# Kernel tuning notes

Hardware: AMD Instinct MI355X
Metric: run time of the kernel (lower is better)

## Reference

```python
import jax, jax.numpy as jnp
import numpy as np

B_, S_, H_, I_, N_, K_ = 2, 2048, 1024, 2048, 16, 4

def setup_inputs() -> dict:
    key = jax.random.key(0)
    ks = jax.random.split(key, 6)
    return {
        "x": jax.random.normal(ks[0], (B_, S_, H_), jnp.float32),
        "W_in": jax.random.normal(ks[1], (H_, 2 * I_), jnp.float32) * (H_ ** -0.5),
        "conv_w": jax.random.normal(ks[2], (I_, 1, K_), jnp.float32) * (K_ ** -0.5),
        "ln_gamma": jnp.ones((I_,), jnp.float32),
        "ln_beta": jnp.zeros((I_,), jnp.float32),
        "W_xproj": jax.random.normal(ks[3], (I_, 2 * N_ + 1), jnp.float32) * (I_ ** -0.5),
        "A_param": jax.random.normal(ks[4], (I_, N_), jnp.float32) * 0.1,
        "D": jnp.ones((I_,), jnp.float32),
        "W_out": jax.random.normal(ks[5], (I_, H_), jnp.float32) * (I_ ** -0.5),
    }

def _layernorm(x, g, b, eps=1e-5):
    mu = jnp.mean(x, axis=-1, keepdims=True)
    var = jnp.mean((x - mu) ** 2, axis=-1, keepdims=True)
    return (x - mu) * jax.lax.rsqrt(var + eps) * g + b

def reference(x, W_in, conv_w, ln_gamma, ln_beta, W_xproj, A_param, D, W_out):
    b, s, _ = x.shape
    n = A_param.shape[1]
    xz = x @ W_in                                   # (b,s,2I)
    xc, z = jnp.split(xz, 2, axis=-1)
    # depthwise causal conv1d: torch pads both sides k-1 then truncates [:s] == left-pad k-1
    xc = jax.lax.conv_general_dilated(
        xc.transpose(0, 2, 1), conv_w, window_strides=(1,),
        padding=[(conv_w.shape[-1] - 1, 0)],
        feature_group_count=conv_w.shape[0],
        dimension_numbers=("NCH", "OIH", "NCH")).transpose(0, 2, 1)  # (b,s,I)
    xc = jax.nn.silu(xc)
    xc = _layernorm(xc, ln_gamma, ln_beta)
    xp = xc @ W_xproj                               # (b,s,2N+1)
    delta = jnp.clip(jax.nn.softplus(xp[..., :1]), 1e-6, 10.0)   # (b,s,1)
    Bm = xp[..., 1:1 + n]                           # (b,s,N)
    Cm = xp[..., 1 + n:]                            # (b,s,N)
    A = -jnp.clip(jax.nn.softplus(A_param), 0.1, 10.0)           # (I,N)
    # decay[b,s,i,n] = exp(delta[b,s] * A[i,n]), clamped
    decay = jnp.clip(jnp.exp(delta[..., None] * A[None, None]), 1e-6, 1.0)  # (b,s,I,N)
    # y = x * sum_n B*C*decay  (state-dim reduction of the broadcast 4D tensor)
    y = xc * jnp.einsum("bsn,bsin->bsi", Bm * Cm, decay)
    y = y + xc * D
    return (y * jax.nn.silu(z)) @ W_out
```

## Files before the change

### kernel.cpp

```cpp
#include <hip/hip_runtime.h>
#include <hip/hip_bf16.h>
#include <cmath>

typedef __bf16 bf16_t;
typedef __bf16 bf16x8 __attribute__((ext_vector_type(8)));
typedef __bf16 bf16x4 __attribute__((ext_vector_type(4)));
typedef float  f32x4  __attribute__((ext_vector_type(4)));

static constexpr int B_  = 2, S_ = 2048, H_ = 1024, I_ = 2048, NST = 16;
static constexpr int ROWS  = B_ * S_;
static constexpr int TWO_I = 2 * I_;
static constexpr int XPD   = 2 * NST + 1;
static constexpr int XPN   = 64;

#define AS_G(p) ((const __attribute__((address_space(1))) void*)(p))
#define AS_L(p) ((__attribute__((address_space(3))) void*)(p))

template<int N> __device__ __forceinline__ void wait_vmcnt();
template<> __device__ __forceinline__ void wait_vmcnt<4>() {
    asm volatile("s_waitcnt vmcnt(4)" ::: "memory");
}

__device__ __forceinline__ float softplus_f(float x) {
    return x > 15.f ? x : log1pf(__expf(x));
}

__device__ __forceinline__ f32x4 b2f(bf16x4 v) {
    return (f32x4){(float)v[0], (float)v[1], (float)v[2], (float)v[3]};
}

__device__ __forceinline__ float fast_exp2(float x) {
#if __has_builtin(__builtin_amdgcn_exp2f)
    return __builtin_amdgcn_exp2f(x);
#else
    return exp2f(x);
#endif
}
__device__ __forceinline__ float fast_rcp(float x) {
#if __has_builtin(__builtin_amdgcn_rcpf)
    return __builtin_amdgcn_rcpf(x);
#else
    return 1.f / x;
#endif
}
__device__ __forceinline__ float fast_sigmoid(float x) {
    return fast_rcp(1.f + __expf(-x));
}
__device__ __forceinline__ float rflf(float x) {
    return __int_as_float(__builtin_amdgcn_readfirstlane(__float_as_int(x)));
}

template<int GX, int GY, int XW>
__device__ __forceinline__ void xcd_swz(int id, int& bx, int& by) {
    constexpr int SX = GX / XW;
    constexpr int SY = GY * XW / 8;
    const int xcd = id & 7;
    const int j   = id >> 3;
    bx = (xcd % XW) * SX + j % SX;
    by = (xcd / XW) * SY + j / SX;
}


__global__ __launch_bounds__(256)
void prep_all(const float* __restrict__ x, const float* __restrict__ W_in,
              const float* __restrict__ W_out, const float* __restrict__ A_param,
              const float* __restrict__ Wx, const float* __restrict__ conv_w,
              bf16_t* __restrict__ Xb, bf16_t* __restrict__ W1t,
              bf16_t* __restrict__ Wot, float* __restrict__ A2T,
              float* __restrict__ cwT, bf16_t* __restrict__ WxTb)
{
    const int b   = blockIdx.x;
    const int tid = threadIdx.x;
    __shared__ float t[32][33];

    if (b < 4096) {
        const int i = b * 256 + tid;
        f32x4 v = *(const f32x4*)(x + (size_t)i * 4);
        bf16x4 o;
        o[0] = (bf16_t)v[0]; o[1] = (bf16_t)v[1];
        o[2] = (bf16_t)v[2]; o[3] = (bf16_t)v[3];
        *(bf16x4*)(Xb + (size_t)i * 4) = o;
    } else if (b < 8192) {
        const int tb = b - 4096;
        const int c0 = (tb & 127) * 32, r0 = (tb >> 7) * 32;
        const int tx = tid & 31, ty = tid >> 5;
        #pragma unroll
        for (int k = 0; k < 4; ++k)
            t[ty + 8 * k][tx] = W_in[(size_t)(r0 + ty + 8 * k) * 4096 + c0 + tx];
        __syncthreads();
        #pragma unroll
        for (int k = 0; k < 4; ++k)
            W1t[(size_t)(c0 + ty + 8 * k) * 1024 + r0 + tx] = (bf16_t)t[tx][ty + 8 * k];
    } else if (b < 10240) {
        const int tb = b - 8192;
        const int c0 = (tb & 31) * 32, r0 = (tb >> 5) * 32;
        const int tx = tid & 31, ty = tid >> 5;
        #pragma unroll
        for (int k = 0; k < 4; ++k)
            t[ty + 8 * k][tx] = W_out[(size_t)(r0 + ty + 8 * k) * 1024 + c0 + tx];
        __syncthreads();
        #pragma unroll
        for (int k = 0; k < 4; ++k)
            Wot[(size_t)(c0 + ty + 8 * k) * 2048 + r0 + tx] = (bf16_t)t[tx][ty + 8 * k];
    } else {
        const int i = (b - 10240) * 256 + tid;
        if (i < NST * I_) {
            int n = i >> 11, c = i & (I_ - 1);
            float sp = softplus_f(A_param[(size_t)c * NST + n]);
            A2T[i] = -fminf(fmaxf(sp, 0.1f), 10.f) * 1.44269504088896340736f;
        }
        if (i < 4 * I_) {
            int j = i >> 11, c = i & (I_ - 1);
            cwT[i] = conv_w[(size_t)c * 4 + j];
        }
        if (i < XPN * I_) {
            int j = i >> 11, c = i & (I_ - 1);
            WxTb[i] = (j < XPD) ? (bf16_t)Wx[(size_t)c * XPD + j] : (bf16_t)0.f;
        }
    }
}


template<int M, int N, int K, int BM, int BN, int WM, int WN, int THREADS,
         int GX, int GY, int XW, typename OutT>
__global__ __launch_bounds__(THREADS)
void gemm_fp(const bf16_t* __restrict__ A, const bf16_t* __restrict__ Bt,
             OutT* __restrict__ C)
{
    constexpr int BK  = 32;
    constexpr int NT  = K / BK;
    constexpr int MR  = BM / WM / 16;
    constexpr int NR  = BN / WN / 16;
    constexpr int MH  = MR / 2;
    constexpr int RPC = THREADS / 4;
    constexpr int CA  = BM / RPC;
    constexpr int CB  = BN / RPC;
    static_assert(CA + CB == 4, "vmcnt template fixed at 4");

    __shared__ bf16_t lA[4][BM * BK];
    __shared__ bf16_t lB[4][BN * BK];

    int bx, by;
    xcd_swz<GX, GY, XW>(blockIdx.x, bx, by);
    const int bm = by * BM;
    const int bn = bx * BN;

    const int tid  = threadIdx.x;
    const int lane = tid & 63;
    const int wave = tid >> 6;
    const int wm   = wave / WN;
    const int wn   = wave % WN;

    const int frow = lane & 15;
    const int fsw  = ((lane >> 4) ^ ((frow >> 1) & 3)) << 3;

    const int str = tid >> 2;
    const int stp = tid & 3;

    const bf16_t* baseA[CA];
    #pragma unroll
    for (int a = 0; a < CA; ++a) {
        const int rt = a * RPC + str;
        baseA[a] = A + (size_t)(bm + rt) * K + ((stp ^ ((rt >> 1) & 3)) << 3);
    }
    const bf16_t* baseB[CB];
    #pragma unroll
    for (int a = 0; a < CB; ++a) {
        const int rt = a * RPC + str;
        baseB[a] = Bt + (size_t)(bn + rt) * K + ((stp ^ ((rt >> 1) & 3)) << 3);
    }

    f32x4 acc[MR][NR];
    #pragma unroll
    for (int m = 0; m < MR; ++m)
        #pragma unroll
        for (int n = 0; n < NR; ++n)
            acc[m][n] = (f32x4){0.f, 0.f, 0.f, 0.f};

    auto stageA = [&](int k0, int b) {
        #pragma unroll
        for (int a = 0; a < CA; ++a)
            __builtin_amdgcn_global_load_lds(AS_G(baseA[a] + k0),
                AS_L(&lA[b][a * RPC * 32 + wave * 512]), 16, 0, 0);
    };
    auto stageB = [&](int k0, int b) {
        #pragma unroll
        for (int a = 0; a < CB; ++a)
            __builtin_amdgcn_global_load_lds(AS_G(baseB[a] + k0),
                AS_L(&lB[b][a * RPC * 32 + wave * 512]), 16, 0, 0);
    };

    stageA(0, 0); stageB(0, 0);
    stageA(BK, 1); stageB(BK, 1);
    wait_vmcnt<4>();
    __builtin_amdgcn_s_barrier();

    #pragma unroll 1
    for (int t = 0; t < NT; ++t) {
        const int buf = t & 3;
        const int nb  = (t + 2) & 3;
        int kn = (t + 2) * BK;
        if (kn >= K) kn -= K;

        bf16x8 bfr[NR];
        #pragma unroll
        for (int n = 0; n < NR; ++n)
            bfr[n] = *(const bf16x8*)(&lB[buf][(wn * (NR * 16) + n * 16 + frow) * 32 + fsw]);
        bf16x8 af0[MH];
        #pragma unroll
        for (int m = 0; m < MH; ++m)
            af0[m] = *(const bf16x8*)(&lA[buf][(wm * (MR * 16) + m * 16 + frow) * 32 + fsw]);
        stageA(kn, nb);

        __builtin_amdgcn_s_setprio(1);
        #pragma unroll
        for (int m = 0; m < MH; ++m)
            #pragma unroll
            for (int n = 0; n < NR; ++n)
                acc[m][n] = __builtin_amdgcn_mfma_f32_16x16x32_bf16(
                    af0[m], bfr[n], acc[m][n], 0, 0, 0);
        __builtin_amdgcn_s_setprio(0);

        bf16x8 af1[MR - MH];
        #pragma unroll
        for (int m = 0; m < MR - MH; ++m)
            af1[m] = *(const bf16x8*)(&lA[buf][(wm * (MR * 16) + (MH + m) * 16 + frow) * 32 + fsw]);
        stageB(kn, nb);

        __builtin_amdgcn_s_setprio(1);
        #pragma unroll
        for (int m = 0; m < MR - MH; ++m)
            #pragma unroll
            for (int n = 0; n < NR; ++n)
                acc[MH + m][n] = __builtin_amdgcn_mfma_f32_16x16x32_bf16(
                    af1[m], bfr[n], acc[MH + m][n], 0, 0, 0);
        __builtin_amdgcn_s_setprio(0);

        wait_vmcnt<4>();
        __builtin_amdgcn_s_barrier();
    }

    const int crow = (lane >> 4) * 4;
    const int ccol = lane & 15;
    #pragma unroll
    for (int m = 0; m < MR; ++m)
        #pragma unroll
        for (int n = 0; n < NR; ++n)
            #pragma unroll
            for (int r = 0; r < 4; ++r)
                C[(size_t)(bm + wm * (MR * 16) + m * 16 + crow + r) * N
                  + (bn + wn * (NR * 16) + n * 16 + ccol)] = (OutT)acc[m][n][r];
}


template<int M, int N, int K, int GX, int GY, int XW>
__global__ __launch_bounds__(512)
void gemm3_kg(const bf16_t* __restrict__ A, const bf16_t* __restrict__ Bt,
              float* __restrict__ C)
{
    constexpr int BM = 128, BN = 128, BK = 32;
    constexpr int KH = K / 2;
    constexpr int NT = KH / BK;
    constexpr int MR = 4, NR = 4, MH = 2;

    __shared__ bf16_t smem[65536];

    int bx, by;
    xcd_swz<GX, GY, XW>(blockIdx.x, bx, by);
    const int bm = by * BM;
    const int bn = bx * BN;

    const int tid  = threadIdx.x;
    const int lane = tid & 63;
    const int wave = tid >> 6;
    const int grp  = wave >> 2;
    const int gw   = wave & 3;
    const int wm   = gw >> 1;
    const int wn   = gw & 1;

    const int frow = lane & 15;
    const int fsw  = ((lane >> 4) ^ ((frow >> 1) & 3)) << 3;

    const int gtid = tid & 255;
    const int str  = gtid >> 2;
    const int stp  = gtid & 3;

    bf16_t* lA = smem + grp * 16384;
    bf16_t* lB = smem + 32768 + grp * 16384;

    const bf16_t* baseA[2];
    #pragma unroll
    for (int a = 0; a < 2; ++a) {
        const int rt = a * 64 + str;
        baseA[a] = A + (size_t)(bm + rt) * K + grp * KH + ((stp ^ ((rt >> 1) & 3)) << 3);
    }
    const bf16_t* baseB[2];
    #pragma unroll
    for (int a = 0; a < 2; ++a) {
        const int rt = a * 64 + str;
        baseB[a] = Bt + (size_t)(bn + rt) * K + grp * KH + ((stp ^ ((rt >> 1) & 3)) << 3);
    }

    f32x4 acc[MR][NR];
    #pragma unroll
    for (int m = 0; m < MR; ++m)
        #pragma unroll
        for (int n = 0; n < NR; ++n)
            acc[m][n] = (f32x4){0.f, 0.f, 0.f, 0.f};

    auto stageA = [&](int k0, int b) {
        #pragma unroll
        for (int a = 0; a < 2; ++a)
            __builtin_amdgcn_global_load_lds(AS_G(baseA[a] + k0),
                AS_L(lA + b * 4096 + a * 2048 + gw * 512), 16, 0, 0);
    };
    auto stageB = [&](int k0, int b) {
        #pragma unroll
        for (int a = 0; a < 2; ++a)
            __builtin_amdgcn_global_load_lds(AS_G(baseB[a] + k0),
                AS_L(lB + b * 4096 + a * 2048 + gw * 512), 16, 0, 0);
    };

    stageA(0, 0); stageB(0, 0);
    stageA(BK, 1); stageB(BK, 1);
    wait_vmcnt<4>();
    __builtin_amdgcn_s_barrier();

    #pragma unroll 1
    for (int t = 0; t < NT; ++t) {
        const int buf = t & 3;
        const int nb  = (t + 2) & 3;
        int kn = (t + 2) * BK;
        if (kn >= KH) kn -= KH;

        bf16x8 bfr[NR];
        #pragma unroll
        for (int n = 0; n < NR; ++n)
            bfr[n] = *(const bf16x8*)(lB + buf * 4096 + (wn * 64 + n * 16 + frow) * 32 + fsw);
        bf16x8 af0[MH];
        #pragma unroll
        for (int m = 0; m < MH; ++m)
            af0[m] = *(const bf16x8*)(lA + buf * 4096 + (wm * 64 + m * 16 + frow) * 32 + fsw);
        stageA(kn, nb);

        __builtin_amdgcn_s_setprio(1);
        #pragma unroll
        for (int m = 0; m < MH; ++m)
            #pragma unroll
            for (int n = 0; n < NR; ++n)
                acc[m][n] = __builtin_amdgcn_mfma_f32_16x16x32_bf16(
                    af0[m], bfr[n], acc[m][n], 0, 0, 0);
        __builtin_amdgcn_s_setprio(0);

        bf16x8 af1[MR - MH];
        #pragma unroll
        for (int m = 0; m < MR - MH; ++m)
            af1[m] = *(const bf16x8*)(lA + buf * 4096 + (wm * 64 + (MH + m) * 16 + frow) * 32 + fsw);
        stageB(kn, nb);

        __builtin_amdgcn_s_setprio(1);
        #pragma unroll
        for (int m = 0; m < MR - MH; ++m)
            #pragma unroll
            for (int n = 0; n < NR; ++n)
                acc[MH + m][n] = __builtin_amdgcn_mfma_f32_16x16x32_bf16(
                    af1[m], bfr[n], acc[MH + m][n], 0, 0, 0);
        __builtin_amdgcn_s_setprio(0);

        wait_vmcnt<4>();
        __builtin_amdgcn_s_barrier();
    }

    asm volatile("s_waitcnt vmcnt(0)" ::: "memory");
    __builtin_amdgcn_s_barrier();

    float* accx = (float*)smem;
    const int crow = (lane >> 4) * 4;
    const int ccol = lane & 15;

    if (grp == 1) {
        #pragma unroll
        for (int m = 0; m < MR; ++m)
            #pragma unroll
            for (int n = 0; n < NR; ++n) {
                const int row = wm * 64 + m * 16 + crow;
                const int col = wn * 64 + n * 16 + ccol;
                #pragma unroll
                for (int r = 0; r < 4; ++r)
                    accx[(size_t)(row + r) * 132 + col] = acc[m][n][r];
            }
    }
    __syncthreads();
    if (grp == 0) {
        #pragma unroll
        for (int m = 0; m < MR; ++m)
            #pragma unroll
            for (int n = 0; n < NR; ++n) {
                const int row = wm * 64 + m * 16 + crow;
                const int col = wn * 64 + n * 16 + ccol;
                #pragma unroll
                for (int r = 0; r < 4; ++r)
                    C[(size_t)(bm + row + r) * N + bn + col] =
                        acc[m][n][r] + accx[(size_t)(row + r) * 132 + col];
            }
    }
}


__global__ __launch_bounds__(256)
void conv_ln(const bf16_t* __restrict__ xz,
             const float* __restrict__ cwT,
             const float* __restrict__ ln_g,
             const float* __restrict__ ln_b,
             bf16_t* __restrict__ Xn)
{
    const int row  = blockIdx.x;
    const int s    = row & (S_ - 1);
    const int tid  = threadIdx.x;
    const int lane = tid & 63;
    const int wave = tid >> 6;
    const bf16_t* xzr = xz + (size_t)row * TWO_I;

    __shared__ float lnr[4][2];

    float xc[8];
    float sm = 0.f, sq = 0.f;

    #pragma unroll
    for (int g = 0; g < 2; ++g) {
        const int c = g * 1024 + tid * 4;
        const f32x4 w0 = *(const f32x4*)(cwT + 0 * I_ + c);
        const f32x4 w1 = *(const f32x4*)(cwT + 1 * I_ + c);
        const f32x4 w2 = *(const f32x4*)(cwT + 2 * I_ + c);
        const f32x4 w3 = *(const f32x4*)(cwT + 3 * I_ + c);
        const f32x4 z4 = (f32x4){0.f, 0.f, 0.f, 0.f};
        const f32x4 xv0 = (s >= 3) ? b2f(*(const bf16x4*)(xzr - 3 * TWO_I + c)) : z4;
        const f32x4 xv1 = (s >= 2) ? b2f(*(const bf16x4*)(xzr - 2 * TWO_I + c)) : z4;
        const f32x4 xv2 = (s >= 1) ? b2f(*(const bf16x4*)(xzr - 1 * TWO_I + c)) : z4;
        const f32x4 xv3 = b2f(*(const bf16x4*)(xzr + c));
        const f32x4 a = w0 * xv0 + w1 * xv1 + w2 * xv2 + w3 * xv3;
        #pragma unroll
        for (int e = 0; e < 4; ++e) {
            const float v = a[e];
            const float t = v * fast_sigmoid(v);
            xc[g * 4 + e] = t;
            sm += t; sq += t * t;
        }
    }

    #pragma unroll
    for (int off = 32; off; off >>= 1) {
        sm += __shfl_xor(sm, off, 64);
        sq += __shfl_xor(sq, off, 64);
    }
    if (lane == 0) { lnr[wave][0] = sm; lnr[wave][1] = sq; }
    __syncthreads();
    sm = lnr[0][0] + lnr[1][0] + lnr[2][0] + lnr[3][0];
    sq = lnr[0][1] + lnr[1][1] + lnr[2][1] + lnr[3][1];
    const float mu = sm * (1.f / I_);
    const float rs = rsqrtf(sq * (1.f / I_) - mu * mu + 1e-5f);

    #pragma unroll
    for (int g = 0; g < 2; ++g) {
        const int c = g * 1024 + tid * 4;
        const f32x4 gg = *(const f32x4*)(ln_g + c);
        const f32x4 bb = *(const f32x4*)(ln_b + c);
        bf16x4 h4;
        #pragma unroll
        for (int e = 0; e < 4; ++e)
            h4[e] = (bf16_t)((xc[g * 4 + e] - mu) * rs * gg[e] + bb[e]);
        *(bf16x4*)(Xn + (size_t)row * I_ + c) = h4;
    }
}


__global__ __launch_bounds__(256)
void xproj_gemm(const bf16_t* __restrict__ Xn,
                const bf16_t* __restrict__ Wb, float* __restrict__ xp_part)
{
    constexpr int BM = 128, BK = 32, KS = 512;
    __shared__ bf16_t lA[BM * BK];
    __shared__ bf16_t lB[XPN * BK];

    const int bm   = blockIdx.x * BM;
    const int ks   = blockIdx.y;
    const int tid  = threadIdx.x;
    const int lane = tid & 63;
    const int wave = tid >> 6;
    const int wm   = (wave >> 1) * 64;
    const int wn   = (wave & 1) * 32;

    const int srow  = lane >> 2;
    const int skoff = (lane & 3) * 8;
    const int frow  = lane & 15;
    const int fko   = (lane >> 4) * 8;

    f32x4 acc[4][2];
    #pragma unroll
    for (int m = 0; m < 4; ++m)
        #pragma unroll
        for (int n = 0; n < 2; ++n)
            acc[m][n] = (f32x4){0.f, 0.f, 0.f, 0.f};

    for (int k0 = ks * KS; k0 < ks * KS + KS; k0 += BK) {
        #pragma unroll
        for (int t = 0; t < 2; ++t) {
            const int c = wave * 2 + t;
            const bf16_t* ga = Xn + (size_t)(bm + c * 16 + srow) * I_ + k0 + skoff;
            __builtin_amdgcn_global_load_lds(AS_G(ga), AS_L(lA + c * 512), 16, 0, 0);
        }
        const bf16_t* gb = Wb + (size_t)(wave * 16 + srow) * I_ + k0 + skoff;
        __builtin_amdgcn_global_load_lds(AS_G(gb), AS_L(lB + wave * 512), 16, 0, 0);
        __syncthreads();

        bf16x8 af[4], bf2[2];
        #pragma unroll
        for (int m = 0; m < 4; ++m)
            af[m] = *(const bf16x8*)(lA + (wm + m * 16 + frow) * BK + fko);
        #pragma unroll
        for (int n = 0; n < 2; ++n)
            bf2[n] = *(const bf16x8*)(lB + (wn + n * 16 + frow) * BK + fko);

        #pragma unroll
        for (int m = 0; m < 4; ++m)
            #pragma unroll
            for (int n = 0; n < 2; ++n)
                acc[m][n] = __builtin_amdgcn_mfma_f32_16x16x32_bf16(
                    af[m], bf2[n], acc[m][n], 0, 0, 0);

        __syncthreads();
    }

    float* out = xp_part + ((size_t)ks * ROWS + bm) * XPN;
    const int crow = (lane >> 4) * 4;
    const int ccol = lane & 15;
    #pragma unroll
    for (int m = 0; m < 4; ++m)
        #pragma unroll
        for (int n = 0; n < 2; ++n)
            #pragma unroll
            for (int r = 0; r < 4; ++r)
                out[(size_t)(wm + m * 16 + crow + r) * XPN
                    + (wn + n * 16 + ccol)] = acc[m][n][r];
}


__global__ __launch_bounds__(256)
void ssm_gate(const bf16_t* __restrict__ xz,
              const bf16_t* __restrict__ Xn,
              const float* __restrict__ xp_part,
              const float* __restrict__ A2T,
              const float* __restrict__ Dv,
              bf16_t* __restrict__ U)
{
    const int row0 = blockIdx.x * 2;
    const int tid  = threadIdx.x;

    __shared__ float xps[2][XPD];
    __shared__ float bcs[2][NST];

    if (tid < XPD) {
        float s = 0.f;
        #pragma unroll
        for (int ks = 0; ks < 4; ++ks)
            s += xp_part[((size_t)ks * ROWS + row0) * XPN + tid];
        xps[0][tid] = s;
    } else if (tid >= 64 && tid < 64 + XPD) {
        const int j = tid - 64;
        float s = 0.f;
        #pragma unroll
        for (int ks = 0; ks < 4; ++ks)
            s += xp_part[((size_t)ks * ROWS + row0 + 1) * XPN + j];
        xps[1][j] = s;
    }
    __syncthreads();
    if (tid < NST)
        bcs[0][tid] = xps[0][1 + tid] * xps[0][1 + NST + tid];
    else if (tid >= 64 && tid < 64 + NST) {
        const int n = tid - 64;
        bcs[1][n] = xps[1][1 + n] * xps[1][1 + NST + n];
    }
    __syncthreads();

    const float d0 = fminf(fmaxf(softplus_f(xps[0][0]), 1e-6f), 10.f);
    const float d1 = fminf(fmaxf(softplus_f(xps[1][0]), 1e-6f), 10.f);

    const bf16_t* z0 = xz + (size_t)row0 * TWO_I + I_;
    const bf16_t* z1 = z0 + TWO_I;
    bf16_t* u0 = U + (size_t)row0 * I_;
    bf16_t* u1 = u0 + I_;

    #pragma unroll 1
    for (int g = 0; g < 2; ++g) {
        const int c = g * 1024 + tid * 4;
        f32x4 sa0 = (f32x4){0.f, 0.f, 0.f, 0.f};
        f32x4 sa1 = (f32x4){0.f, 0.f, 0.f, 0.f};
        #pragma unroll 1
        for (int nb = 0; nb < 4; ++nb) {
            const float* ap = A2T + (size_t)(nb * 4) * I_ + c;
            const f32x4 a0 = *(const f32x4*)(ap);
            const f32x4 a1 = *(const f32x4*)(ap + I_);
            const f32x4 a2 = *(const f32x4*)(ap + 2 * I_);
            const f32x4 a3 = *(const f32x4*)(ap + 3 * I_);
            const float b00 = rflf(bcs[0][nb * 4 + 0]), b10 = rflf(bcs[1][nb * 4 + 0]);
            const float b01 = rflf(bcs[0][nb * 4 + 1]), b11 = rflf(bcs[1][nb * 4 + 1]);
            const float b02 = rflf(bcs[0][nb * 4 + 2]), b12 = rflf(bcs[1][nb * 4 + 2]);
            const float b03 = rflf(bcs[0][nb * 4 + 3]), b13 = rflf(bcs[1][nb * 4 + 3]);
            #pragma unroll
            for (int e = 0; e < 4; ++e) {
                sa0[e] += b00 * fast_exp2(d0 * a0[e]);
                sa1[e] += b10 * fast_exp2(d1 * a0[e]);
                sa0[e] += b01 * fast_exp2(d0 * a1[e]);
                sa1[e] += b11 * fast_exp2(d1 * a1[e]);
                sa0[e] += b02 * fast_exp2(d0 * a2[e]);
                sa1[e] += b12 * fast_exp2(d1 * a2[e]);
                sa0[e] += b03 * fast_exp2(d0 * a3[e]);
                sa1[e] += b13 * fast_exp2(d1 * a3[e]);
            }
        }
        const f32x4 dvv = *(const f32x4*)(Dv + c);
        const f32x4 xn0 = b2f(*(const bf16x4*)(Xn + (size_t)row0 * I_ + c));
        const f32x4 xn1 = b2f(*(const bf16x4*)(Xn + (size_t)(row0 + 1) * I_ + c));
        const f32x4 zv0 = b2f(*(const bf16x4*)(z0 + c));
        const f32x4 zv1 = b2f(*(const bf16x4*)(z1 + c));
        bf16x4 o0, o1;
        #pragma unroll
        for (int e = 0; e < 4; ++e) {
            const float y0 = xn0[e] * (sa0[e] + dvv[e]);
            const float y1 = xn1[e] * (sa1[e] + dvv[e]);
            const float zz0 = zv0[e], zz1 = zv1[e];
            o0[e] = (bf16_t)(y0 * zz0 * fast_sigmoid(zz0));
            o1[e] = (bf16_t)(y1 * zz1 * fast_sigmoid(zz1));
        }
        *(bf16x4*)(u0 + c) = o0;
        *(bf16x4*)(u1 + c) = o1;
    }
}


extern "C" void kernel_launch(void* const* d_in, const int* in_sizes, int n_in,
                              void* d_out, int out_size, void* d_ws, size_t ws_size,
                              hipStream_t stream)
{
    const float* x     = (const float*)d_in[0];
    const float* W_in  = (const float*)d_in[1];
    const float* convw = (const float*)d_in[2];
    const float* ln_g  = (const float*)d_in[3];
    const float* ln_b  = (const float*)d_in[4];
    const float* Wx    = (const float*)d_in[5];
    const float* A_p   = (const float*)d_in[6];
    const float* Dv    = (const float*)d_in[7];
    const float* W_out = (const float*)d_in[8];
    float* out = (float*)d_out;

    char* ws = (char*)d_ws;
    bf16_t* Xb   = (bf16_t*)(ws);
    bf16_t* W1t  = (bf16_t*)(ws + (size_t)(8u  << 20));
    bf16_t* Wot  = (bf16_t*)(ws + (size_t)(16u << 20));
    float*  A2T  = (float*) (ws + (size_t)(20u << 20));
    float*  cwT  = (float*) (ws + (size_t)(20u << 20) + (128u << 10));
    bf16_t* WxTb = (bf16_t*)(ws + (size_t)(20u << 20) + (256u << 10));
    bf16_t* XZb  = (bf16_t*)(ws + (size_t)(22u << 20));
    bf16_t* U    = (bf16_t*)(ws + (size_t)(54u << 20));
    bf16_t* Xn   = (bf16_t*)(ws);
    float*  xp4  = (float*) (ws + (size_t)(86u << 20));

    prep_all<<<10752, 256, 0, stream>>>(x, W_in, W_out, A_p, Wx, convw,
                                        Xb, W1t, Wot, A2T, cwT, WxTb);

    gemm_fp<ROWS, TWO_I, H_, 128, 128, 2, 2, 256, 32, 32, 4, bf16_t>
        <<<1024, 256, 0, stream>>>(Xb, W1t, XZb);
    conv_ln<<<ROWS, 256, 0, stream>>>(XZb, cwT, ln_g, ln_b, Xn);
    xproj_gemm<<<dim3(ROWS / 128, 4), 256, 0, stream>>>(Xn, WxTb, xp4);
    ssm_gate<<<ROWS / 2, 256, 0, stream>>>(XZb, Xn, xp4, A2T, Dv, U);
    gemm3_kg<ROWS, H_, I_, 8, 32, 2>
        <<<256, 512, 0, stream>>>(U, Wot, out);
}
```

Baseline: 135.5 us.

## Replace pipelined first GEMM with single-buffered synchronous-load variant

The first projection GEMM drops its 4-deep LDS ring buffer, the prefetch two tiles ahead, the split MFMA phases and the setprio hints. It now loads each K tile into a single LDS buffer, syncs, computes all 16 MFMAs, then syncs again. This cuts LDS use per block from 64KB to 16KB, which can allow more resident blocks per CU, but load/compute overlap inside the block is lost and there are two barriers per iteration.

Measured after the change: 135.9 us. Within noise of the previous version (+0.3%).

```diff
diff --git a/kernel.cpp b/kernel.cpp
--- a/kernel.cpp
+++ b/kernel.cpp
@@ -121,24 +121,17 @@
 }
 
 
-template<int M, int N, int K, int BM, int BN, int WM, int WN, int THREADS,
-         int GX, int GY, int XW, typename OutT>
-__global__ __launch_bounds__(THREADS)
-void gemm_fp(const bf16_t* __restrict__ A, const bf16_t* __restrict__ Bt,
-             OutT* __restrict__ C)
+template<int M, int N, int K, int GX, int GY, int XW>
+__global__ __launch_bounds__(256)
+void gemm1_m97(const bf16_t* __restrict__ A, const bf16_t* __restrict__ Bt,
+               bf16_t* __restrict__ C)
 {
-    constexpr int BK  = 32;
-    constexpr int NT  = K / BK;
-    constexpr int MR  = BM / WM / 16;
-    constexpr int NR  = BN / WN / 16;
-    constexpr int MH  = MR / 2;
-    constexpr int RPC = THREADS / 4;
-    constexpr int CA  = BM / RPC;
-    constexpr int CB  = BN / RPC;
-    static_assert(CA + CB == 4, "vmcnt template fixed at 4");
-
-    __shared__ bf16_t lA[4][BM * BK];
-    __shared__ bf16_t lB[4][BN * BK];
+    constexpr int BM = 128, BN = 128, BK = 32;
+    constexpr int NT = K / BK;
+    constexpr int MR = 4, NR = 4;
+
+    __shared__ bf16_t lA[BM * BK];
+    __shared__ bf16_t lB[BN * BK];
 
     int bx, by;
     xcd_swz<GX, GY, XW>(blockIdx.x, bx, by);
@@ -148,8 +141,8 @@
     const int tid  = threadIdx.x;
     const int lane = tid & 63;
     const int wave = tid >> 6;
-    const int wm   = wave / WN;
-    const int wn   = wave % WN;
+    const int wm   = wave >> 1;
+    const int wn   = wave & 1;
 
     const int frow = lane & 15;
     const int fsw  = ((lane >> 4) ^ ((frow >> 1) & 3)) << 3;
@@ -157,17 +150,14 @@
     const int str = tid >> 2;
     const int stp = tid & 3;
 
-    const bf16_t* baseA[CA];
-    #pragma unroll
-    for (int a = 0; a < CA; ++a) {
-        const int rt = a * RPC + str;
-        baseA[a] = A + (size_t)(bm + rt) * K + ((stp ^ ((rt >> 1) & 3)) << 3);
-    }
-    const bf16_t* baseB[CB];
-    #pragma unroll
-    for (int a = 0; a < CB; ++a) {
-        const int rt = a * RPC + str;
-        baseB[a] = Bt + (size_t)(bn + rt) * K + ((stp ^ ((rt >> 1) & 3)) << 3);
+    const bf16_t* baseA[2];
+    const bf16_t* baseB[2];
+    #pragma unroll
+    for (int a = 0; a < 2; ++a) {
+        const int rt = a * 64 + str;
+        const int ksw = (stp ^ ((rt >> 1) & 3)) << 3;
+        baseA[a] = A  + (size_t)(bm + rt) * K + ksw;
+        baseB[a] = Bt + (size_t)(bn + rt) * K + ksw;
     }
 
     f32x4 acc[MR][NR];
@@ -177,67 +167,33 @@
         for (int n = 0; n < NR; ++n)
             acc[m][n] = (f32x4){0.f, 0.f, 0.f, 0.f};
 
-    auto stageA = [&](int k0, int b) {
-        #pragma unroll
-        for (int a = 0; a < CA; ++a)
+    for (int t = 0; t < NT; ++t) {
+        const int k0 = t * BK;
+        #pragma unroll
+        for (int a = 0; a < 2; ++a) {
             __builtin_amdgcn_global_load_lds(AS_G(baseA[a] + k0),
-                AS_L(&lA[b][a * RPC * 32 + wave * 512]), 16, 0, 0);
-    };
-    auto stageB = [&](int k0, int b) {
-        #pragma unroll
-        for (int a = 0; a < CB; ++a)
+                AS_L(lA + a * 2048 + wave * 512), 16, 0, 0);
             __builtin_amdgcn_global_load_lds(AS_G(baseB[a] + k0),
-                AS_L(&lB[b][a * RPC * 32 + wave * 512]), 16, 0, 0);
-    };
-
-    stageA(0, 0); stageB(0, 0);
-    stageA(BK, 1); stageB(BK, 1);
-    wait_vmcnt<4>();
-    __builtin_amdgcn_s_barrier();
-
-    #pragma unroll 1
-    for (int t = 0; t < NT; ++t) {
-        const int buf = t & 3;
-        const int nb  = (t + 2) & 3;
-        int kn = (t + 2) * BK;
-        if (kn >= K) kn -= K;
-
-        bf16x8 bfr[NR];
+                AS_L(lB + a * 2048 + wave * 512), 16, 0, 0);
+        }
+        __syncthreads();
+
+        bf16x8 af[MR], bfr[NR];
+        #pragma unroll
+        for (int m = 0; m < MR; ++m)
+            af[m] = *(const bf16x8*)(lA + (wm * 64 + m * 16 + frow) * 32 + fsw);
         #pragma unroll
         for (int n = 0; n < NR; ++n)
-            bfr[n] = *(const bf16x8*)(&lB[buf][(wn * (NR * 16) + n * 16 + frow) * 32 + fsw]);
-        bf16x8 af0[MH];
-        #pragma unroll
-        for (int m = 0; m < MH; ++m)
-            af0[m] = *(const bf16x8*)(&lA[buf][(wm * (MR * 16) + m * 16 + frow) * 32 + fsw]);
-        stageA(kn, nb);
-
-        __builtin_amdgcn_s_setprio(1);
-        #pragma unroll
-        for (int m = 0; m < MH; ++m)
+            bfr[n] = *(const bf16x8*)(lB + (wn * 64 + n * 16 + frow) * 32 + fsw);
+
+        #pragma unroll
+        for (int m = 0; m < MR; ++m)
             #pragma unroll
             for (int n = 0; n < NR; ++n)
                 acc[m][n] = __builtin_amdgcn_mfma_f32_16x16x32_bf16(
-                    af0[m], bfr[n], acc[m][n], 0, 0, 0);
-        __builtin_amdgcn_s_setprio(0);
-
-        bf16x8 af1[MR - MH];
-        #pragma unroll
-        for (int m = 0; m < MR - MH; ++m)
-            af1[m] = *(const bf16x8*)(&lA[buf][(wm * (MR * 16) + (MH + m) * 16 + frow) * 32 + fsw]);
-        stageB(kn, nb);
-
-        __builtin_amdgcn_s_setprio(1);
-        #pragma unroll
-        for (int m = 0; m < MR - MH; ++m)
-            #pragma unroll
-            for (int n = 0; n < NR; ++n)
-                acc[MH + m][n] = __builtin_amdgcn_mfma_f32_16x16x32_bf16(
-                    af1[m], bfr[n], acc[MH + m][n], 0, 0, 0);
-        __builtin_amdgcn_s_setprio(0);
-
-        wait_vmcnt<4>();
-        __builtin_amdgcn_s_barrier();
+                    af[m], bfr[n], acc[m][n], 0, 0, 0);
+
+        __syncthreads();
     }
 
     const int crow = (lane >> 4) * 4;
@@ -248,8 +204,8 @@
         for (int n = 0; n < NR; ++n)
             #pragma unroll
             for (int r = 0; r < 4; ++r)
-                C[(size_t)(bm + wm * (MR * 16) + m * 16 + crow + r) * N
-                  + (bn + wn * (NR * 16) + n * 16 + ccol)] = (OutT)acc[m][n][r];
+                C[(size_t)(bm + wm * 64 + m * 16 + crow + r) * N
+                  + (bn + wn * 64 + n * 16 + ccol)] = (bf16_t)acc[m][n][r];
 }
 
 
@@ -668,7 +624,7 @@
     prep_all<<<10752, 256, 0, stream>>>(x, W_in, W_out, A_p, Wx, convw,
                                         Xb, W1t, Wot, A2T, cwT, WxTb);
 
-    gemm_fp<ROWS, TWO_I, H_, 128, 128, 2, 2, 256, 32, 32, 4, bf16_t>
+    gemm1_m97<ROWS, TWO_I, H_, 32, 32, 4>
         <<<1024, 256, 0, stream>>>(Xb, W1t, XZb);
     conv_ln<<<ROWS, 256, 0, stream>>>(XZb, cwT, ln_g, ln_b, Xn);
     xproj_gemm<<<dim3(ROWS / 128, 4), 256, 0, stream>>>(Xn, WxTb, xp4);
```
